# Optimization experiments

Hardware: AMD Instinct MI355X
Metric: run time of the kernel (lower is better)

Reference implementation:

```python
import jax, jax.numpy as jnp
import numpy as np

D_MODEL = 1024
NUM_HEADS = 16
D_K = D_MODEL // NUM_HEADS
B, S = 1, 4096


def setup_inputs() -> dict:
    key = jax.random.key(0)
    ks = jax.random.split(key, 11)
    std = 1.0 / np.sqrt(D_MODEL)
    def lin(k):
        kw, kb = jax.random.split(k)
        W = jax.random.uniform(kw, (D_MODEL, D_MODEL), jnp.float32, -std, std)
        b = jax.random.uniform(kb, (D_MODEL,), jnp.float32, -std, std)
        return W, b
    Wq, bq = lin(ks[0]); Wk, bk = lin(ks[1]); Wv, bv = lin(ks[2]); Wo, bo = lin(ks[3])
    q = jax.random.normal(ks[4], (B, S, D_MODEL), jnp.float32)
    k = jax.random.normal(ks[5], (B, S, D_MODEL), jnp.float32)
    v = jax.random.normal(ks[6], (B, S, D_MODEL), jnp.float32)
    return {"q": q, "k": k, "v": v,
            "Wq": Wq, "bq": bq, "Wk": Wk, "bk": bk,
            "Wv": Wv, "bv": bv, "Wo": Wo, "bo": bo}


def reference(q, k, v, Wq, bq, Wk, bk, Wv, bv, Wo, bo):
    Bq, Sq, _ = q.shape
    # Linear projections (torch Linear: x @ W.T + b)
    def split_heads(x):
        return x.reshape(Bq, -1, NUM_HEADS, D_K).transpose(0, 2, 1, 3)  # [B,H,S,Dk]
    query = split_heads(q @ Wq.T + bq)
    key_ = split_heads(k @ Wk.T + bk)
    value = split_heads(v @ Wv.T + bv)
    scores = jnp.einsum('bhsd,bhtd->bhst', query, key_) / jnp.sqrt(jnp.float32(D_K))
    attn = jax.nn.softmax(scores, axis=-1)  # [B,H,S,S]
    ctx = jnp.einsum('bhst,bhtd->bhsd', attn, value)
    ctx = ctx.transpose(0, 2, 1, 3).reshape(Bq, Sq, NUM_HEADS * D_K)
    return ctx @ Wo.T + bo
```

## Files before the change

kernel.cpp:

```cpp
#include <hip/hip_runtime.h>
#include <cstdint>
#include <cstddef>

#define S_LEN 4096
#define DMODEL 1024
#define NHEADS 16
#define DK 64
#define ACT (S_LEN * DMODEL)
#define WELE (DMODEL * DMODEL)

typedef __bf16 bf16;
typedef bf16  bf16x2 __attribute__((ext_vector_type(2)));
typedef bf16  bf16x4 __attribute__((ext_vector_type(4)));
typedef bf16  bf16x8 __attribute__((ext_vector_type(8)));
typedef float f32x4  __attribute__((ext_vector_type(4)));
typedef float f32x16 __attribute__((ext_vector_type(16)));
typedef unsigned int uint32x4v __attribute__((ext_vector_type(4)));

__device__ __forceinline__ void async16(const void* g, void* l) {
    __builtin_amdgcn_global_load_lds(
        (__attribute__((address_space(1))) void*)(uintptr_t)g,
        (__attribute__((address_space(3))) void*)(uintptr_t)l,
        16, 0, 0);
}

__device__ __forceinline__ float fast_exp2(float x) {
#if __has_builtin(__builtin_amdgcn_exp2f)
    return __builtin_amdgcn_exp2f(x);
#else
    return exp2f(x);
#endif
}

__device__ __forceinline__ unsigned pk2(float a, float b) {
    bf16x2 t; t[0] = (bf16)a; t[1] = (bf16)b;
    return __builtin_bit_cast(unsigned, t);
}

__device__ __forceinline__ void pl32swap(unsigned &a, unsigned &b) {
    asm volatile("v_permlane32_swap_b32 %0, %1" : "+v"(a), "+v"(b));
}

__device__ __forceinline__ bf16x8 mkfrag(unsigned w0, unsigned w1, unsigned w2, unsigned w3) {
    uint32x4v u = { w0, w1, w2, w3 };
    return __builtin_bit_cast(bf16x8, u);
}

__global__ void __launch_bounds__(256) cvt7(
    const float* a0, const float* a1, const float* a2,
    const float* w0, const float* w1, const float* w2, const float* w3,
    bf16* oa0, bf16* oa1, bf16* oa2,
    bf16* ow0, bf16* ow1, bf16* ow2, bf16* ow3,
    int nA, int nB)
{
    const float* s; bf16* d; int n4;
    switch (blockIdx.y) {
        case 0: s = a0; d = oa0; n4 = nA; break;
        case 1: s = a1; d = oa1; n4 = nA; break;
        case 2: s = a2; d = oa2; n4 = nA; break;
        case 3: s = w0; d = ow0; n4 = nB; break;
        case 4: s = w1; d = ow1; n4 = nB; break;
        case 5: s = w2; d = ow2; n4 = nB; break;
        default: s = w3; d = ow3; n4 = nB; break;
    }
    int i = blockIdx.x * 256 + threadIdx.x;
    if (i < n4) {
        float4 v = ((const float4*)s)[i];
        bf16x4 r = { (bf16)v.x, (bf16)v.y, (bf16)v.z, (bf16)v.w };
        ((bf16x4*)d)[i] = r;
    }
}

__device__ __forceinline__ void gemm_compute_128(
    const bf16* As, const bf16* Bs, f32x4 (&acc)[4][4],
    int wm, int wn, int l16, int quad)
{
    bf16x8 af[4], bfr[4];
#pragma unroll
    for (int i = 0; i < 4; ++i)
        af[i] = *(const bf16x8*)&As[(wm + i * 16 + l16) * 32 + quad * 8];
#pragma unroll
    for (int i = 0; i < 4; ++i)
        bfr[i] = *(const bf16x8*)&Bs[(wn + i * 16 + l16) * 32 + quad * 8];
#pragma unroll
    for (int mi = 0; mi < 4; ++mi)
#pragma unroll
        for (int ni = 0; ni < 4; ++ni)
            acc[mi][ni] = __builtin_amdgcn_mfma_f32_16x16x32_bf16(
                af[mi], bfr[ni], acc[mi][ni], 0, 0, 0);
}

__device__ __forceinline__ void gemm_core_bk64(
    const bf16* __restrict__ A, const bf16* __restrict__ B,
    bf16* As, bf16* Bs, f32x4 (&acc)[4][4],
    int m0, int n0, int wm, int wn, int K)
{
    const int tid  = threadIdx.x;
    const int wave = tid >> 6;
    const int lane = tid & 63;
    const int quad = lane >> 4;
    const int l16  = lane & 15;

    const int srow = tid >> 2;
    const int scol = (tid & 3) * 8;
    const bf16* Ag = A + (size_t)(m0 + srow) * K + scol;
    const bf16* Bg = B + (size_t)(n0 + srow) * K + scol;
    char* lA = (char*)As + wave * 1024;
    char* lB = (char*)Bs + wave * 1024;

    for (int k0 = 0; k0 < K; k0 += 64) {
        async16(Ag,                       lA);
        async16(Ag + (size_t)64 * K,      lA + 4096);
        async16(Ag + 32,                  lA + 8192);
        async16(Ag + 32 + (size_t)64 * K, lA + 12288);
        async16(Bg,                       lB);
        async16(Bg + (size_t)64 * K,      lB + 4096);
        async16(Bg + 32,                  lB + 8192);
        async16(Bg + 32 + (size_t)64 * K, lB + 12288);
        Ag += 64; Bg += 64;
        __syncthreads();

        gemm_compute_128(As,        Bs,        acc, wm, wn, l16, quad);
        gemm_compute_128(As + 4096, Bs + 4096, acc, wm, wn, l16, quad);
        __syncthreads();
    }
}

__global__ void __launch_bounds__(256) proj_qkv(
    const bf16* __restrict__ Xq, const bf16* __restrict__ Wq, const float* __restrict__ bq, bf16* __restrict__ Qo,
    const bf16* __restrict__ Xk, const bf16* __restrict__ Wk, const float* __restrict__ bk, bf16* __restrict__ Ko,
    const bf16* __restrict__ Xv, const bf16* __restrict__ Wv, const float* __restrict__ bv, bf16* __restrict__ Vo,
    float qscale)
{
    __shared__ __align__(16) bf16 As[2 * 128 * 32];
    __shared__ __align__(16) bf16 Bs[2 * 128 * 32];

    const int which = blockIdx.z;
    const bf16*  A    = (which == 0) ? Xq : (which == 1) ? Xk : Xv;
    const bf16*  Bw   = (which == 0) ? Wq : (which == 1) ? Wk : Wv;
    const float* bias = (which == 0) ? bq : (which == 1) ? bk : bv;
    const float  scale = (which == 0) ? qscale : 1.0f;

    const int tid  = threadIdx.x;
    const int wave = tid >> 6;
    const int lane = tid & 63;
    const int quad = lane >> 4;
    const int l16  = lane & 15;
    const int m0 = blockIdx.x * 128;
    const int n0 = blockIdx.y * 128;
    const int wm = (wave & 1) * 64;
    const int wn = (wave >> 1) * 64;

    f32x4 acc[4][4] = {};
    gemm_core_bk64(A, Bw, As, Bs, acc, m0, n0, wm, wn, DMODEL);

    if (which < 2) {
        bf16* out = (which == 0) ? Qo : Ko;
#pragma unroll
        for (int mi = 0; mi < 4; ++mi)
#pragma unroll
            for (int ni = 0; ni < 4; ++ni) {
                const int n = n0 + wn + ni * 16 + l16;
                const float bn = bias[n];
                const int dk = n & 63;
                const int cc = dk >> 3, ee = dk & 7;
                const size_t hb = (size_t)(n >> 6) * S_LEN * DK;
#pragma unroll
                for (int r = 0; r < 4; ++r) {
                    const int m = m0 + wm + mi * 16 + quad * 4 + r;
                    const int pdk = ((cc ^ (m & 7)) << 3) | ee;
                    out[hb + (size_t)m * DK + pdk] = (bf16)((acc[mi][ni][r] + bn) * scale);
                }
            }
    } else {
#pragma unroll
        for (int mi = 0; mi < 4; ++mi)
#pragma unroll
            for (int ni = 0; ni < 4; ++ni) {
                const int n = n0 + wn + ni * 16 + l16;
                const float bn = bias[n];
                const int dk = n & 63;
                const size_t hb = (size_t)(n >> 6) * (64 * S_LEN);
                const int mbase = m0 + wm + mi * 16 + quad * 4;
                const int T  = mbase >> 6;
                const int tt = mbase & 63;
                const int pos = (((tt >> 3) ^ (dk & 7)) << 3) | (tt & 7);
                bf16x4 r4;
#pragma unroll
                for (int r = 0; r < 4; ++r) r4[r] = (bf16)(acc[mi][ni][r] + bn);
                *(bf16x4*)&Vo[hb + (size_t)T * 4096 + dk * 64 + pos] = r4;
            }
    }
}

__global__ void __launch_bounds__(256) gemm_out(
    const bf16* __restrict__ A, const bf16* __restrict__ Bw,
    const float* __restrict__ bias, float* __restrict__ out)
{
    __shared__ __align__(16) bf16 As[64 * 32];
    __shared__ __align__(16) bf16 Bs[128 * 32];

    const int tid  = threadIdx.x;
    const int wave = tid >> 6;
    const int lane = tid & 63;
    const int quad = lane >> 4;
    const int l16  = lane & 15;
    const int m0 = blockIdx.x * 64;
    const int n0 = blockIdx.y * 128;
    const int wm = (wave & 1) * 32;
    const int wn = (wave >> 1) * 64;

    const int srow = tid >> 2;
    const int scol = (tid & 3) * 8;
    const bf16* Ag  = A  + (size_t)(m0 + srow) * DMODEL + scol;
    const bf16* Bg  = Bw + (size_t)(n0 + srow) * DMODEL + scol;
    const bf16* Bg2 = Bg + (size_t)64 * DMODEL;

    f32x4 acc[2][4] = {};
    for (int k0 = 0; k0 < DMODEL; k0 += 32) {
        async16(Ag,  (char*)As + wave * 1024);
        async16(Bg,  (char*)Bs + wave * 1024);
        async16(Bg2, (char*)Bs + 4096 + wave * 1024);
        Ag += 32; Bg += 32; Bg2 += 32;
        __syncthreads();

        bf16x8 af[2], bfr[4];
#pragma unroll
        for (int i = 0; i < 2; ++i)
            af[i] = *(const bf16x8*)&As[(wm + i * 16 + l16) * 32 + quad * 8];
#pragma unroll
        for (int i = 0; i < 4; ++i)
            bfr[i] = *(const bf16x8*)&Bs[(wn + i * 16 + l16) * 32 + quad * 8];

#pragma unroll
        for (int mi = 0; mi < 2; ++mi)
#pragma unroll
            for (int ni = 0; ni < 4; ++ni)
                acc[mi][ni] = __builtin_amdgcn_mfma_f32_16x16x32_bf16(
                    af[mi], bfr[ni], acc[mi][ni], 0, 0, 0);
        __syncthreads();
    }

#pragma unroll
    for (int mi = 0; mi < 2; ++mi)
#pragma unroll
        for (int ni = 0; ni < 4; ++ni) {
            const int n = n0 + wn + ni * 16 + l16;
            const float bn = bias[n];
#pragma unroll
            for (int r = 0; r < 4; ++r) {
                const int m = m0 + wm + mi * 16 + quad * 4 + r;
                out[(size_t)m * DMODEL + n] = acc[mi][ni][r] + bn;
            }
        }
}

__global__ void __launch_bounds__(256) flash_attn(
    const bf16* __restrict__ Q, const bf16* __restrict__ Kh,
    const bf16* __restrict__ Vt, bf16* __restrict__ ctx)
{
    __shared__ __align__(16) bf16 Qs[128 * 64];
    __shared__ __align__(16) bf16 Ks[2][64 * 64];
    __shared__ __align__(16) bf16 Vs[2][64 * 64];

    const int tid  = threadIdx.x;
    const int wave = tid >> 6;
    const int lane = tid & 63;
    const int l31  = lane & 31;
    const int hi   = lane >> 5;
    const int x7   = lane & 7;
    const int s0 = blockIdx.x * 128;
    const int h  = blockIdx.y;

    const bf16* Kg = Kh + (size_t)h * S_LEN * DK + tid * 8;
    const bf16* Vg = Vt + (size_t)h * (64 * S_LEN) + tid * 8;

    {
        const bf16* Qg = Q + (size_t)h * S_LEN * DK + (size_t)s0 * DK + tid * 8;
#pragma unroll
        for (int j = 0; j < 4; ++j)
            async16(Qg + j * 2048, (char*)Qs + j * 4096 + wave * 1024);
    }
    async16(Kg,        (char*)Ks + wave * 1024);
    async16(Kg + 2048, (char*)Ks + 4096 + wave * 1024);
    async16(Vg,        (char*)Vs + wave * 1024);
    async16(Vg + 2048, (char*)Vs + 4096 + wave * 1024);
    Kg += 4096; Vg += 4096;
    __syncthreads();

    bf16x8 qf[4];
    {
        const bf16* qb = &Qs[(wave * 32 + l31) * 64];
#pragma unroll
        for (int ks = 0; ks < 4; ++ks)
            qf[ks] = *(const bf16x8*)(qb + ((((ks << 1) + hi) ^ x7) << 3));
    }

    f32x16 od[2] = {};
    float lsum = 0.0f;
    int cur = 0;

    for (int it = 0; it < 64; ++it) {
        if (it < 63) {
            char* lK = (char*)Ks + (cur ^ 1) * 8192 + wave * 1024;
            char* lV = (char*)Vs + (cur ^ 1) * 8192 + wave * 1024;
            async16(Kg,        lK);
            async16(Kg + 2048, lK + 4096);
            async16(Vg,        lV);
            async16(Vg + 2048, lV + 4096);
            Kg += 4096; Vg += 4096;
        }
        const bf16* Kc = &Ks[cur][0];
        const bf16* Vc = &Vs[cur][0];

        f32x16 st[2] = {};
        __builtin_amdgcn_s_setprio(1);
#pragma unroll
        for (int tt = 0; tt < 2; ++tt) {
            const bf16* kb = &Kc[(tt * 32 + l31) * 64];
#pragma unroll
            for (int ks = 0; ks < 4; ++ks) {
                bf16x8 kf = *(const bf16x8*)(kb + ((((ks << 1) + hi) ^ x7) << 3));
                st[tt] = __builtin_amdgcn_mfma_f32_32x32x16_bf16(kf, qf[ks], st[tt], 0, 0, 0);
            }
        }
        __builtin_amdgcn_s_setprio(0);

        bf16x8 pf[4];
#pragma unroll
        for (int tt = 0; tt < 2; ++tt) {
            float p[16];
#pragma unroll
            for (int r = 0; r < 16; ++r) {
                p[r] = fast_exp2(st[tt][r]);
                lsum += p[r];
            }
#pragma unroll
            for (int w = 0; w < 2; ++w) {
                const int G = w * 8;
                unsigned A0 = pk2(p[G + 0], p[G + 1]);
                unsigned A1 = pk2(p[G + 2], p[G + 3]);
                unsigned B0 = pk2(p[G + 4], p[G + 5]);
                unsigned B1 = pk2(p[G + 6], p[G + 7]);
                pl32swap(A0, B0);
                pl32swap(A1, B1);
                pf[tt * 2 + w] = mkfrag(A0, A1, B0, B1);
            }
        }

        __builtin_amdgcn_s_setprio(1);
#pragma unroll
        for (int dd = 0; dd < 2; ++dd) {
            const bf16* vb = &Vc[(dd * 32 + l31) * 64];
#pragma unroll
            for (int ks = 0; ks < 4; ++ks) {
                bf16x8 vf = *(const bf16x8*)(vb + ((((ks << 1) + hi) ^ x7) << 3));
                od[dd] = __builtin_amdgcn_mfma_f32_32x32x16_bf16(vf, pf[ks], od[dd], 0, 0, 0);
            }
        }
        __builtin_amdgcn_s_setprio(0);

        __syncthreads();
        cur ^= 1;
    }

    lsum += __shfl_xor(lsum, 32);
    const float rinv = 1.0f / lsum;
    const int s = s0 + wave * 32 + l31;
#pragma unroll
    for (int dd = 0; dd < 2; ++dd)
#pragma unroll
        for (int g = 0; g < 4; ++g) {
            bf16x4 r4;
#pragma unroll
            for (int r = 0; r < 4; ++r)
                r4[r] = (bf16)(od[dd][g * 4 + r] * rinv);
            *(bf16x4*)&ctx[(size_t)s * DMODEL + h * DK + dd * 32 + g * 8 + hi * 4] = r4;
        }
}

extern "C" void kernel_launch(void* const* d_in, const int* in_sizes, int n_in,
                              void* d_out, int out_size, void* d_ws, size_t ws_size,
                              hipStream_t stream)
{
    (void)in_sizes; (void)n_in; (void)out_size; (void)ws_size;
    const float* q  = (const float*)d_in[0];
    const float* k  = (const float*)d_in[1];
    const float* v  = (const float*)d_in[2];
    const float* Wq = (const float*)d_in[3];
    const float* bq = (const float*)d_in[4];
    const float* Wk = (const float*)d_in[5];
    const float* bk = (const float*)d_in[6];
    const float* Wv = (const float*)d_in[7];
    const float* bv = (const float*)d_in[8];
    const float* Wo = (const float*)d_in[9];
    const float* bo = (const float*)d_in[10];

    bf16* Xq  = (bf16*)d_ws;
    bf16* Xk  = Xq  + ACT;
    bf16* Xv  = Xk  + ACT;
    bf16* Wqb = Xv  + ACT;
    bf16* Wkb = Wqb + WELE;
    bf16* Wvb = Wkb + WELE;
    bf16* Wob = Wvb + WELE;
    bf16* Qh  = Wob + WELE;
    bf16* Kh  = Qh  + ACT;
    bf16* Vt  = Kh  + ACT;
    bf16* CTX = Vt  + ACT;

    cvt7<<<dim3(ACT / 4 / 256, 7), 256, 0, stream>>>(
        q, k, v, Wq, Wk, Wv, Wo,
        Xq, Xk, Xv, Wqb, Wkb, Wvb, Wob, ACT / 4, WELE / 4);

    const float qscale = 0.125f * 1.4426950408889634f;
    proj_qkv<<<dim3(S_LEN / 128, DMODEL / 128, 3), 256, 0, stream>>>(
        Xq, Wqb, bq, Qh, Xk, Wkb, bk, Kh, Xv, Wvb, bv, Vt, qscale);

    flash_attn<<<dim3(S_LEN / 128, NHEADS), 256, 0, stream>>>(Qh, Kh, Vt, CTX);

    gemm_out<<<dim3(S_LEN / 64, DMODEL / 128), 256, 0, stream>>>(CTX, Wob, bo, (float*)d_out);
}
```

Baseline: 269.0 us.

## Double queries per attention block and split keys across two partial passes

Each flash-attention wave now processes two 32-row query groups, so a block covers 256 queries and every K/V tile in LDS feeds twice as many MFMAs. The key range is split in two across blockIdx.z, keeping the grid at 512 blocks. Unnormalized fp32 partial outputs and row sums go to reused workspace buffers, and a new combine kernel adds the halves, normalizes and writes bf16 context for the output GEMM. This trades less LDS/global K-V traffic per query for higher register pressure, extra fp32 partial traffic and an additional kernel launch.

```diff
diff --git a/kernel.cpp b/kernel.cpp
--- a/kernel.cpp
+++ b/kernel.cpp
@@ -255,11 +255,13 @@
         }
 }
 
-__global__ void __launch_bounds__(256) flash_attn(
+__global__ void __launch_bounds__(256, 2) flash_attn(
     const bf16* __restrict__ Q, const bf16* __restrict__ Kh,
-    const bf16* __restrict__ Vt, bf16* __restrict__ ctx)
-{
-    __shared__ __align__(16) bf16 Qs[128 * 64];
+    const bf16* __restrict__ Vt,
+    float* __restrict__ O0, float* __restrict__ O1lo, float* __restrict__ O1hi,
+    float* __restrict__ lsums)
+{
+    __shared__ __align__(16) bf16 Qs[256 * 64];
     __shared__ __align__(16) bf16 Ks[2][64 * 64];
     __shared__ __align__(16) bf16 Vs[2][64 * 64];
 
@@ -269,16 +271,17 @@
     const int l31  = lane & 31;
     const int hi   = lane >> 5;
     const int x7   = lane & 7;
-    const int s0 = blockIdx.x * 128;
+    const int s0 = blockIdx.x * 256;
     const int h  = blockIdx.y;
-
-    const bf16* Kg = Kh + (size_t)h * S_LEN * DK + tid * 8;
-    const bf16* Vg = Vt + (size_t)h * (64 * S_LEN) + tid * 8;
+    const int z  = blockIdx.z;
+
+    const bf16* Kg = Kh + (size_t)h * S_LEN * DK + (size_t)z * 2048 * DK + tid * 8;
+    const bf16* Vg = Vt + (size_t)h * (64 * S_LEN) + (size_t)z * 32 * 4096 + tid * 8;
 
     {
         const bf16* Qg = Q + (size_t)h * S_LEN * DK + (size_t)s0 * DK + tid * 8;
 #pragma unroll
-        for (int j = 0; j < 4; ++j)
+        for (int j = 0; j < 8; ++j)
             async16(Qg + j * 2048, (char*)Qs + j * 4096 + wave * 1024);
     }
     async16(Kg,        (char*)Ks + wave * 1024);
@@ -288,20 +291,21 @@
     Kg += 4096; Vg += 4096;
     __syncthreads();
 
-    bf16x8 qf[4];
-    {
-        const bf16* qb = &Qs[(wave * 32 + l31) * 64];
+    bf16x8 qf[2][4];
+#pragma unroll
+    for (int g = 0; g < 2; ++g) {
+        const bf16* qb = &Qs[(wave * 64 + g * 32 + l31) * 64];
 #pragma unroll
         for (int ks = 0; ks < 4; ++ks)
-            qf[ks] = *(const bf16x8*)(qb + ((((ks << 1) + hi) ^ x7) << 3));
-    }
-
-    f32x16 od[2] = {};
-    float lsum = 0.0f;
+            qf[g][ks] = *(const bf16x8*)(qb + ((((ks << 1) + hi) ^ x7) << 3));
+    }
+
+    f32x16 od[2][2] = {};
+    float lsum[2] = {};
     int cur = 0;
 
-    for (int it = 0; it < 64; ++it) {
-        if (it < 63) {
+    for (int it = 0; it < 32; ++it) {
+        if (it < 31) {
             char* lK = (char*)Ks + (cur ^ 1) * 8192 + wave * 1024;
             char* lV = (char*)Vs + (cur ^ 1) * 8192 + wave * 1024;
             async16(Kg,        lK);
@@ -313,7 +317,7 @@
         const bf16* Kc = &Ks[cur][0];
         const bf16* Vc = &Vs[cur][0];
 
-        f32x16 st[2] = {};
+        f32x16 st[2][2] = {};
         __builtin_amdgcn_s_setprio(1);
 #pragma unroll
         for (int tt = 0; tt < 2; ++tt) {
@@ -321,32 +325,35 @@
 #pragma unroll
             for (int ks = 0; ks < 4; ++ks) {
                 bf16x8 kf = *(const bf16x8*)(kb + ((((ks << 1) + hi) ^ x7) << 3));
-                st[tt] = __builtin_amdgcn_mfma_f32_32x32x16_bf16(kf, qf[ks], st[tt], 0, 0, 0);
+                st[0][tt] = __builtin_amdgcn_mfma_f32_32x32x16_bf16(kf, qf[0][ks], st[0][tt], 0, 0, 0);
+                st[1][tt] = __builtin_amdgcn_mfma_f32_32x32x16_bf16(kf, qf[1][ks], st[1][tt], 0, 0, 0);
             }
         }
         __builtin_amdgcn_s_setprio(0);
 
-        bf16x8 pf[4];
-#pragma unroll
-        for (int tt = 0; tt < 2; ++tt) {
-            float p[16];
-#pragma unroll
-            for (int r = 0; r < 16; ++r) {
-                p[r] = fast_exp2(st[tt][r]);
-                lsum += p[r];
-            }
-#pragma unroll
-            for (int w = 0; w < 2; ++w) {
-                const int G = w * 8;
-                unsigned A0 = pk2(p[G + 0], p[G + 1]);
-                unsigned A1 = pk2(p[G + 2], p[G + 3]);
-                unsigned B0 = pk2(p[G + 4], p[G + 5]);
-                unsigned B1 = pk2(p[G + 6], p[G + 7]);
-                pl32swap(A0, B0);
-                pl32swap(A1, B1);
-                pf[tt * 2 + w] = mkfrag(A0, A1, B0, B1);
-            }
-        }
+        bf16x8 pf[2][4];
+#pragma unroll
+        for (int g = 0; g < 2; ++g)
+#pragma unroll
+            for (int tt = 0; tt < 2; ++tt) {
+                float p[16];
+#pragma unroll
+                for (int r = 0; r < 16; ++r) {
+                    p[r] = fast_exp2(st[g][tt][r]);
+                    lsum[g] += p[r];
+                }
+#pragma unroll
+                for (int w = 0; w < 2; ++w) {
+                    const int G = w * 8;
+                    unsigned A0 = pk2(p[G + 0], p[G + 1]);
+                    unsigned A1 = pk2(p[G + 2], p[G + 3]);
+                    unsigned B0 = pk2(p[G + 4], p[G + 5]);
+                    unsigned B1 = pk2(p[G + 6], p[G + 7]);
+                    pl32swap(A0, B0);
+                    pl32swap(A1, B1);
+                    pf[g][tt * 2 + w] = mkfrag(A0, A1, B0, B1);
+                }
+            }
 
         __builtin_amdgcn_s_setprio(1);
 #pragma unroll
@@ -355,7 +362,8 @@
 #pragma unroll
             for (int ks = 0; ks < 4; ++ks) {
                 bf16x8 vf = *(const bf16x8*)(vb + ((((ks << 1) + hi) ^ x7) << 3));
-                od[dd] = __builtin_amdgcn_mfma_f32_32x32x16_bf16(vf, pf[ks], od[dd], 0, 0, 0);
+                od[0][dd] = __builtin_amdgcn_mfma_f32_32x32x16_bf16(vf, pf[0][ks], od[0][dd], 0, 0, 0);
+                od[1][dd] = __builtin_amdgcn_mfma_f32_32x32x16_bf16(vf, pf[1][ks], od[1][dd], 0, 0, 0);
             }
         }
         __builtin_amdgcn_s_setprio(0);
@@ -364,19 +372,41 @@
         cur ^= 1;
     }
 
-    lsum += __shfl_xor(lsum, 32);
-    const float rinv = 1.0f / lsum;
-    const int s = s0 + wave * 32 + l31;
-#pragma unroll
-    for (int dd = 0; dd < 2; ++dd)
-#pragma unroll
-        for (int g = 0; g < 4; ++g) {
-            bf16x4 r4;
-#pragma unroll
-            for (int r = 0; r < 4; ++r)
-                r4[r] = (bf16)(od[dd][g * 4 + r] * rinv);
-            *(bf16x4*)&ctx[(size_t)s * DMODEL + h * DK + dd * 32 + g * 8 + hi * 4] = r4;
-        }
+    float* Ob = (z == 0) ? O0
+              : (s0 < 2048 ? O1lo : O1hi - (size_t)2048 * DMODEL);
+    float* lz = lsums + (size_t)z * S_LEN * NHEADS;
+#pragma unroll
+    for (int g = 0; g < 2; ++g) {
+        float ls = lsum[g] + __shfl_xor(lsum[g], 32);
+        const int s = s0 + wave * 64 + g * 32 + l31;
+        if (hi == 0) lz[s * NHEADS + h] = ls;
+        float* bp = Ob + (size_t)s * DMODEL + h * DK;
+#pragma unroll
+        for (int dd = 0; dd < 2; ++dd)
+#pragma unroll
+            for (int gg = 0; gg < 4; ++gg) {
+                f32x4 r4 = { od[g][dd][gg * 4 + 0], od[g][dd][gg * 4 + 1],
+                             od[g][dd][gg * 4 + 2], od[g][dd][gg * 4 + 3] };
+                *(f32x4*)&bp[dd * 32 + gg * 8 + hi * 4] = r4;
+            }
+    }
+}
+
+__global__ void __launch_bounds__(256) combine(
+    const float* __restrict__ O0, const float* __restrict__ O1lo,
+    const float* __restrict__ O1hi, const float* __restrict__ lsums,
+    bf16* __restrict__ ctxn)
+{
+    const int idx = blockIdx.x * 256 + threadIdx.x;
+    const int s = idx >> 8;
+    float4 a = ((const float4*)O0)[idx];
+    float4 b = (s < 2048) ? ((const float4*)O1lo)[idx]
+                          : ((const float4*)O1hi)[idx - 2048 * 256];
+    const int sh = idx >> 4;
+    const float rinv = 1.0f / (lsums[sh] + lsums[S_LEN * NHEADS + sh]);
+    bf16x4 r = { (bf16)((a.x + b.x) * rinv), (bf16)((a.y + b.y) * rinv),
+                 (bf16)((a.z + b.z) * rinv), (bf16)((a.w + b.w) * rinv) };
+    ((bf16x4*)ctxn)[idx] = r;
 }
 
 extern "C" void kernel_launch(void* const* d_in, const int* in_sizes, int n_in,
@@ -408,6 +438,12 @@
     bf16* Vt  = Kh  + ACT;
     bf16* CTX = Vt  + ACT;
 
+    float* O0    = (float*)Xq;
+    float* O1lo  = (float*)CTX;
+    float* O1hi  = (float*)Xv;
+    float* lsums = (float*)Wkb;
+    bf16*  CTXn  = Qh;
+
     cvt7<<<dim3(ACT / 4 / 256, 7), 256, 0, stream>>>(
         q, k, v, Wq, Wk, Wv, Wo,
         Xq, Xk, Xv, Wqb, Wkb, Wvb, Wob, ACT / 4, WELE / 4);
@@ -416,7 +452,10 @@
     proj_qkv<<<dim3(S_LEN / 128, DMODEL / 128, 3), 256, 0, stream>>>(
         Xq, Wqb, bq, Qh, Xk, Wkb, bk, Kh, Xv, Wvb, bv, Vt, qscale);
 
-    flash_attn<<<dim3(S_LEN / 128, NHEADS), 256, 0, stream>>>(Qh, Kh, Vt, CTX);
-
-    gemm_out<<<dim3(S_LEN / 64, DMODEL / 128), 256, 0, stream>>>(CTX, Wob, bo, (float*)d_out);
-}
+    flash_attn<<<dim3(S_LEN / 256, NHEADS, 2), 256, 0, stream>>>(
+        Qh, Kh, Vt, O0, O1lo, O1hi, lsums);
+
+    combine<<<dim3(ACT / 4 / 256), 256, 0, stream>>>(O0, O1lo, O1hi, lsums, CTXn);
+
+    gemm_out<<<dim3(S_LEN / 64, DMODEL / 128), 256, 0, stream>>>(CTXn, Wob, bo, (float*)d_out);
+}
```

Result: faster. 256.1 us (-4.8%).
